# Optimization experiments

Measured on AMD Instinct MI355X. Metric: run time of the kernel, lower is better.

Reference implementation:

```python
import jax, jax.numpy as jnp
import numpy as np

N_NODES = 50000
N_EDGES = 800000


def setup_inputs() -> dict:
    key = jax.random.key(0)
    ks = jax.random.split(key, 16)
    def W(k, shape, fan_in):
        return jax.random.normal(k, shape, dtype=jnp.float32) / np.sqrt(fan_in)
    return {
        "x": jax.random.normal(ks[0], (N_NODES, 64), dtype=jnp.float32),
        "edge_attr": jax.random.uniform(ks[1], (N_EDGES, 1), dtype=jnp.float32),
        "edge_index": jax.random.randint(ks[2], (2, N_EDGES), 0, N_NODES, dtype=jnp.int64),
        "W_pre1": W(ks[3], (65, 16), 65), "b_pre1": jnp.zeros((16,), jnp.float32),
        "W_net1": W(ks[4], (16, 16), 16), "b_net1": jnp.zeros((16,), jnp.float32),
        "W_out1": W(ks[5], (16, 16), 16), "b_out1": jnp.zeros((16,), jnp.float32),
        "W_pre2": W(ks[6], (17, 16), 17), "b_pre2": jnp.zeros((16,), jnp.float32),
        "W_net2": W(ks[7], (16, 16), 16), "b_net2": jnp.zeros((16,), jnp.float32),
        "W_out2": W(ks[8], (16, 16), 16), "b_out2": jnp.zeros((16,), jnp.float32),
    }


def _mpnn_conv(x, edge_index, edge_attr, Wp, bp, Wn, bn, Wo, bo, activation):
    """Edge-gather MLP + scatter-max aggregation (MpnnConv)."""
    src, dst = edge_index[0], edge_index[1]
    # per-edge message: Linear(concat(x_src, edge_attr)) -> relu -> net (Linear)
    m = jnp.concatenate([x[src], edge_attr], axis=1) @ Wp + bp      # [E, mid]
    m = jax.nn.relu(m)
    m = m @ Wn + bn                                                  # [E, mid]
    # scatter-max to destination nodes; empty segments -> 0
    agg = jax.ops.segment_max(m, dst, num_segments=x.shape[0])      # [N, mid]
    agg = jnp.where(jnp.isfinite(agg), agg, 0.0)
    out = agg @ Wo + bo                                              # [N, out]
    return activation(out) if activation is not None else out


def reference(x, edge_attr, edge_index,
              W_pre1, b_pre1, W_net1, b_net1, W_out1, b_out1,
              W_pre2, b_pre2, W_net2, b_net2, W_out2, b_out2):
    # eval mode: dropout is identity
    h = _mpnn_conv(x, edge_index, edge_attr, W_pre1, b_pre1, W_net1, b_net1,
                   W_out1, b_out1, jax.nn.elu)
    h = jax.nn.elu(h)  # outer F.elu in Net.forward
    h = _mpnn_conv(h, edge_index, edge_attr, W_pre2, b_pre2, W_net2, b_net2,
                   W_out2, b_out2, None)
    return jax.nn.log_softmax(h, axis=1)
```

## Files before the change

kernel.cpp:

```cpp
#include <hip/hip_runtime.h>
#include <math.h>

#define NN 50000
#define NE 800000
#define BSHIFT 7
#define BNODES 128
#define NB 391
#define NBB 200
#define EPB 4000
#define PRE_BLOCKS 196

__device__ __forceinline__ float elu1(float v) {
    return v > 0.0f ? v : expm1f(v);
}

__global__ void setup_kernel(const int* __restrict__ ei, int* __restrict__ HM,
                             const float* __restrict__ x,
                             const float* __restrict__ Wp,
                             const float* __restrict__ bp,
                             float* __restrict__ P1) {
    __shared__ unsigned hist[NB];
    __shared__ float sW[64 * 16];
    __shared__ float sb[16];
    if (blockIdx.x < NBB) {
        for (int i = threadIdx.x; i < NB; i += 256) hist[i] = 0;
        __syncthreads();
        int base = blockIdx.x * EPB;
        for (int i = threadIdx.x; i < EPB; i += 256) {
            int d = ei[NE + base + i];
            atomicAdd(&hist[d >> BSHIFT], 1u);
        }
        __syncthreads();
        for (int b = threadIdx.x; b < NB; b += 256)
            HM[b * NBB + blockIdx.x] = (int)hist[b];
    } else {
        for (int i = threadIdx.x; i < 64 * 16; i += 256) sW[i] = Wp[i];
        if (threadIdx.x < 16) sb[threadIdx.x] = bp[threadIdx.x];
        __syncthreads();
        int n = (blockIdx.x - NBB) * 256 + threadIdx.x;
        if (n >= NN) return;
        float acc[16];
#pragma unroll
        for (int k = 0; k < 16; ++k) acc[k] = sb[k];
        const float4* xr = (const float4*)(x + (size_t)n * 64);
#pragma unroll
        for (int j4 = 0; j4 < 16; ++j4) {
            float4 xv = xr[j4];
            const float* w = &sW[j4 * 4 * 16];
#pragma unroll
            for (int k = 0; k < 16; ++k) acc[k] += xv.x * w[k];
#pragma unroll
            for (int k = 0; k < 16; ++k) acc[k] += xv.y * w[16 + k];
#pragma unroll
            for (int k = 0; k < 16; ++k) acc[k] += xv.z * w[32 + k];
#pragma unroll
            for (int k = 0; k < 16; ++k) acc[k] += xv.w * w[48 + k];
        }
        float4* o = (float4*)(P1 + (size_t)n * 16);
        o[0] = make_float4(acc[0], acc[1], acc[2], acc[3]);
        o[1] = make_float4(acc[4], acc[5], acc[6], acc[7]);
        o[2] = make_float4(acc[8], acc[9], acc[10], acc[11]);
        o[3] = make_float4(acc[12], acc[13], acc[14], acc[15]);
    }
}

__global__ void row_scan_kernel(int* __restrict__ HM, int* __restrict__ rowsum) {
    __shared__ int s[256];
    int t = threadIdx.x, b = blockIdx.x;
    int v = (t < NBB) ? HM[b * NBB + t] : 0;
    s[t] = v;
    __syncthreads();
#pragma unroll
    for (int off = 1; off < 256; off <<= 1) {
        int tmp = (t >= off) ? s[t - off] : 0;
        __syncthreads();
        s[t] += tmp;
        __syncthreads();
    }
    if (t < NBB) HM[b * NBB + t] = s[t] - v;
    if (t == 255) rowsum[b] = s[255];
}

__global__ void scan_rows_kernel(const int* __restrict__ rowsum, int* __restrict__ bstart) {
    __shared__ int s[512];
    int t = threadIdx.x;
    int v = (t < NB) ? rowsum[t] : 0;
    s[t] = v;
    __syncthreads();
#pragma unroll
    for (int off = 1; off < 512; off <<= 1) {
        int tmp = (t >= off) ? s[t - off] : 0;
        __syncthreads();
        s[t] += tmp;
        __syncthreads();
    }
    if (t < NB) bstart[t] = s[t] - v;
    if (t == 511) bstart[NB] = s[511];
}

__global__ void bin2_kernel(const int* __restrict__ ei, const float* __restrict__ ea,
                            const int* __restrict__ HM, const int* __restrict__ bstart,
                            int2* __restrict__ sp1) {
    __shared__ unsigned cur[NB];
    for (int b = threadIdx.x; b < NB; b += 256)
        cur[b] = (unsigned)(bstart[b] + HM[b * NBB + blockIdx.x]);
    __syncthreads();
    int base = blockIdx.x * EPB;
    for (int i = threadIdx.x; i < EPB; i += 256) {
        int e = base + i;
        int d = ei[NE + e];
        int srcv = ei[e];
        int b = d >> BSHIFT;
        int dl = d & (BNODES - 1);
        unsigned pos = atomicAdd(&cur[b], 1u);
        sp1[pos] = make_int2(srcv | (dl << 16), __float_as_int(ea[e]));
    }
}

__global__ void sort_kernel(const int2* __restrict__ sp1,
                            const int* __restrict__ bstart,
                            int2* __restrict__ sp2,
                            int* __restrict__ start) {
    __shared__ unsigned hist[BNODES];
    __shared__ unsigned cur[BNODES];
    __shared__ int s[256];
    int tid = threadIdx.x;
    int b = blockIdx.x;
    int e0 = bstart[b], e1 = bstart[b + 1];
    if (tid < BNODES) hist[tid] = 0;
    __syncthreads();
    for (int i = e0 + tid; i < e1; i += 256) {
        int dl = (sp1[i].x >> 16) & (BNODES - 1);
        atomicAdd(&hist[dl], 1u);
    }
    __syncthreads();
    int v = (tid < BNODES) ? (int)hist[tid] : 0;
    s[tid] = v;
    __syncthreads();
#pragma unroll
    for (int off = 1; off < 256; off <<= 1) {
        int t = (tid >= off) ? s[tid - off] : 0;
        __syncthreads();
        s[tid] += t;
        __syncthreads();
    }
    if (tid < BNODES) {
        int excl = s[tid] - v;
        cur[tid] = (unsigned)excl;
        start[b * BNODES + tid] = e0 + excl;
    }
    __syncthreads();
    for (int i = e0 + tid; i < e1; i += 256) {
        int2 rec = sp1[i];
        int dl = (rec.x >> 16) & (BNODES - 1);
        int pos = e0 + (int)atomicAdd(&cur[dl], 1u);
        sp2[pos] = make_int2(rec.x & 0xFFFF, rec.y);
    }
}

template <int MODE>
__global__ void __launch_bounds__(256, 4)
gather_kernel(const long long* __restrict__ sp,
              const int* __restrict__ start,
              const float* __restrict__ Pin,
              const float* __restrict__ wl,
              const float* __restrict__ Wn,
              const float* __restrict__ bn,
              const float* __restrict__ Wo,
              const float* __restrict__ bo,
              const float* __restrict__ Wpn,
              const float* __restrict__ bpn,
              float* __restrict__ out) {
    __shared__ float swl[16], sbn[16], sbo[16], sbpn[16];
    __shared__ float sWnT[16][17];
    __shared__ float sWo[256], sWpn[256];
    __shared__ float sAgg[32][17];
    int tid = threadIdx.x;
    if (tid < 256) {
        sWnT[tid & 15][tid >> 4] = Wn[tid];
        sWo[tid] = Wo[tid];
        if (MODE == 0) sWpn[tid] = Wpn[tid];
    }
    if (tid < 16) {
        swl[tid] = wl[tid]; sbn[tid] = bn[tid]; sbo[tid] = bo[tid];
        if (MODE == 0) sbpn[tid] = bpn[tid];
    }
    __syncthreads();

    int l  = tid >> 3;
    int g  = tid & 3;
    int hi = (tid >> 2) & 1;
    int n = blockIdx.x * 32 + l;
    bool valid = (n < NN);

    float acc[4] = {-INFINITY, -INFINITY, -INFINITY, -INFINITY};
    int s0 = 0, s1 = 0;
    if (valid) { s0 = start[n]; s1 = start[n + 1]; }

    float wl0 = swl[g * 4 + 0], wl1 = swl[g * 4 + 1],
          wl2 = swl[g * 4 + 2], wl3 = swl[g * 4 + 3];
    float bn0 = sbn[g * 4 + 0], bn1 = sbn[g * 4 + 1],
          bn2 = sbn[g * 4 + 2], bn3 = sbn[g * 4 + 3];
    bool g1 = (g & 1) != 0, g2 = (g & 2) != 0;

    float wreg[64];
#pragma unroll
    for (int c = 0; c < 16; ++c) {
#pragma unroll
        for (int j = 0; j < 4; ++j) wreg[c * 4 + j] = sWnT[c][g * 4 + j];
    }

    int s = s0 + hi;
    while (s < s1) {
        int sB = (s + 2 < s1) ? (s + 2) : s;
        long long rA = sp[s];
        long long rB = sp[sB];
        int srcA = (int)(rA & 0xFFFFFFFFll);
        int srcB = (int)(rB & 0xFFFFFFFFll);
        float4 qA = ((const float4*)(Pin + (size_t)srcA * 16))[g];
        float4 qB = ((const float4*)(Pin + (size_t)srcB * 16))[g];
        float aA = __int_as_float((int)(rA >> 32));
        float aB = __int_as_float((int)(rB >> 32));
        s += 4;

#pragma unroll
        for (int e = 0; e < 2; ++e) {
            float4 cv = e ? qB : qA;
            float a = e ? aB : aA;
            float t0 = fmaxf(fmaf(a, wl0, cv.x), 0.0f);
            float t1 = fmaxf(fmaf(a, wl1, cv.y), 0.0f);
            float t2 = fmaxf(fmaf(a, wl2, cv.z), 0.0f);
            float t3 = fmaxf(fmaf(a, wl3, cv.w), 0.0f);
            float m[16];
#pragma unroll
            for (int c = 0; c < 16; ++c) {
                float o = t0 * wreg[c * 4 + 0];
                o = fmaf(t1, wreg[c * 4 + 1], o);
                o = fmaf(t2, wreg[c * 4 + 2], o);
                o = fmaf(t3, wreg[c * 4 + 3], o);
                m[c] = o;
            }
            float h[8];
#pragma unroll
            for (int c = 0; c < 8; ++c) {
                float send = g2 ? m[c] : m[c + 8];
                float recv = __shfl_xor(send, 2, 64);
                h[c] = (g2 ? m[c + 8] : m[c]) + recv;
            }
            float send, recv, r0, r1, r2, r3;
            send = g1 ? h[0] : h[4]; recv = __shfl_xor(send, 1, 64); r0 = (g1 ? h[4] : h[0]) + recv;
            send = g1 ? h[1] : h[5]; recv = __shfl_xor(send, 1, 64); r1 = (g1 ? h[5] : h[1]) + recv;
            send = g1 ? h[2] : h[6]; recv = __shfl_xor(send, 1, 64); r2 = (g1 ? h[6] : h[2]) + recv;
            send = g1 ? h[3] : h[7]; recv = __shfl_xor(send, 1, 64); r3 = (g1 ? h[7] : h[3]) + recv;
            acc[0] = fmaxf(acc[0], r0 + bn0);
            acc[1] = fmaxf(acc[1], r1 + bn1);
            acc[2] = fmaxf(acc[2], r2 + bn2);
            acc[3] = fmaxf(acc[3], r3 + bn3);
        }
    }
#pragma unroll
    for (int q = 0; q < 4; ++q) acc[q] = fmaxf(acc[q], __shfl_xor(acc[q], 4, 64));

    bool empty = (s1 == s0);
#pragma unroll
    for (int q = 0; q < 4; ++q) sAgg[l][g * 4 + q] = empty ? 0.0f : acc[q];
    __syncthreads();

    if (MODE == 0) {
        float h[4];
#pragma unroll
        for (int q = 0; q < 4; ++q) {
            int c = g * 4 + q;
            float o = sbo[c];
#pragma unroll
            for (int j = 0; j < 16; ++j) o = fmaf(sAgg[l][j], sWo[j * 16 + c], o);
            h[q] = elu1(elu1(o));
        }
        __syncthreads();
        if (hi == 0) {
#pragma unroll
            for (int q = 0; q < 4; ++q) sAgg[l][g * 4 + q] = h[q];
        }
        __syncthreads();
        float p[4];
#pragma unroll
        for (int q = 0; q < 4; ++q) {
            int c = g * 4 + q;
            float o = sbpn[c];
#pragma unroll
            for (int k = 0; k < 16; ++k) o = fmaf(sAgg[l][k], sWpn[k * 16 + c], o);
            p[q] = o;
        }
        if (valid && hi == 0) {
            float4* op = (float4*)(out + (size_t)n * 16 + g * 4);
            *op = make_float4(p[0], p[1], p[2], p[3]);
        }
    } else {
        float oo[4];
#pragma unroll
        for (int q = 0; q < 4; ++q) {
            int c = g * 4 + q;
            float o = sbo[c];
#pragma unroll
            for (int j = 0; j < 16; ++j) o = fmaf(sAgg[l][j], sWo[j * 16 + c], o);
            oo[q] = o;
        }
        __syncthreads();
        if (hi == 0) {
#pragma unroll
            for (int q = 0; q < 4; ++q) sAgg[l][g * 4 + q] = oo[q];
        }
        __syncthreads();
        float mx = -INFINITY;
#pragma unroll
        for (int j = 0; j < 16; ++j) mx = fmaxf(mx, sAgg[l][j]);
        float sum = 0.0f;
#pragma unroll
        for (int j = 0; j < 16; ++j) sum += expf(sAgg[l][j] - mx);
        float ls = logf(sum) + mx;
        if (valid && hi == 0) {
            float4* op = (float4*)(out + (size_t)n * 16 + g * 4);
            *op = make_float4(oo[0] - ls, oo[1] - ls, oo[2] - ls, oo[3] - ls);
        }
    }
}

extern "C" void kernel_launch(void* const* d_in, const int* in_sizes, int n_in,
                              void* d_out, int out_size, void* d_ws, size_t ws_size,
                              hipStream_t stream) {
    const float* x         = (const float*)d_in[0];
    const float* edge_attr = (const float*)d_in[1];
    const int*   edge_index= (const int*)  d_in[2];
    const float* W_pre1 = (const float*)d_in[3];
    const float* b_pre1 = (const float*)d_in[4];
    const float* W_net1 = (const float*)d_in[5];
    const float* b_net1 = (const float*)d_in[6];
    const float* W_out1 = (const float*)d_in[7];
    const float* b_out1 = (const float*)d_in[8];
    const float* W_pre2 = (const float*)d_in[9];
    const float* b_pre2 = (const float*)d_in[10];
    const float* W_net2 = (const float*)d_in[11];
    const float* b_net2 = (const float*)d_in[12];
    const float* W_out2 = (const float*)d_in[13];
    const float* b_out2 = (const float*)d_in[14];

    char* ws = (char*)d_ws;
    int2*  sp1    = (int2*) (ws);
    int2*  sp2    = (int2*) (ws + 6400000);
    float* P1     = (float*)(ws + 12800000);
    float* P2     = (float*)(ws + 16000000);
    int*   HM     = (int*)  (ws + 19200000);
    int*   bstart = (int*)  (ws + 19520000);
    int*   rowsum = (int*)  (ws + 19524000);
    int*   start  = (int*)  (ws + 19528000);

    const int GATH_BLOCKS = (NN + 31) / 32;

    setup_kernel<<<NBB + PRE_BLOCKS, 256, 0, stream>>>(edge_index, HM, x, W_pre1, b_pre1, P1);
    row_scan_kernel<<<NB, 256, 0, stream>>>(HM, rowsum);
    scan_rows_kernel<<<1, 512, 0, stream>>>(rowsum, bstart);
    bin2_kernel<<<NBB, 256, 0, stream>>>(edge_index, edge_attr, HM, bstart, sp1);
    sort_kernel<<<NB, 256, 0, stream>>>(sp1, bstart, sp2, start);

    gather_kernel<0><<<GATH_BLOCKS, 256, 0, stream>>>((const long long*)sp2, start, P1,
        W_pre1 + 64 * 16, W_net1, b_net1, W_out1, b_out1, W_pre2, b_pre2, P2);

    gather_kernel<1><<<GATH_BLOCKS, 256, 0, stream>>>((const long long*)sp2, start, P2,
        W_pre2 + 16 * 16, W_net2, b_net2, W_out2, b_out2, nullptr, nullptr,
        (float*)d_out);
}
```

Baseline: 96.67 us.

## Sort nodes by in-degree within each bin to balance gather warp work

The sort kernel now counting-sorts the 128 nodes of each bin by in-degree, capped at 63, and emits a permutation array along with the CSR start offsets in permuted order. The gather kernels then process nodes in that permuted order, so the lanes sharing a wavefront handle nodes with similar edge counts and fewer lanes sit idle in the edge loop. The cost is extra scans and shared-memory work in the sort, one extra indirection load per node in the gather, and output writes that are now scattered by node id.

```diff
diff --git a/kernel.cpp b/kernel.cpp
--- a/kernel.cpp
+++ b/kernel.cpp
@@ -120,40 +120,76 @@
 __global__ void sort_kernel(const int2* __restrict__ sp1,
                             const int* __restrict__ bstart,
                             int2* __restrict__ sp2,
-                            int* __restrict__ start) {
+                            int* __restrict__ start,
+                            int* __restrict__ perm) {
     __shared__ unsigned hist[BNODES];
+    __shared__ int s[256];
+    __shared__ unsigned dcnt[64];
+    __shared__ unsigned dcur[64];
+    __shared__ int dlof[BNODES];
+    __shared__ int soff[BNODES];
     __shared__ unsigned cur[BNODES];
-    __shared__ int s[256];
+    __shared__ int sdeg[BNODES];
     int tid = threadIdx.x;
     int b = blockIdx.x;
     int e0 = bstart[b], e1 = bstart[b + 1];
     if (tid < BNODES) hist[tid] = 0;
+    if (tid < 64) dcnt[tid] = 0;
     __syncthreads();
     for (int i = e0 + tid; i < e1; i += 256) {
         int dl = (sp1[i].x >> 16) & (BNODES - 1);
         atomicAdd(&hist[dl], 1u);
     }
     __syncthreads();
-    int v = (tid < BNODES) ? (int)hist[tid] : 0;
+    if (tid < BNODES) {
+        int key = min((int)hist[tid], 63);
+        atomicAdd(&dcnt[key], 1u);
+    }
+    __syncthreads();
+    int v = (tid < 64) ? (int)dcnt[tid] : 0;
     s[tid] = v;
     __syncthreads();
 #pragma unroll
-    for (int off = 1; off < 256; off <<= 1) {
-        int t = (tid >= off) ? s[tid - off] : 0;
-        __syncthreads();
-        s[tid] += t;
-        __syncthreads();
-    }
+    for (int off = 1; off < 64; off <<= 1) {
+        int tmp = (tid >= off) ? s[tid - off] : 0;
+        __syncthreads();
+        s[tid] += tmp;
+        __syncthreads();
+    }
+    if (tid < 64) dcur[tid] = (unsigned)(s[tid] - v);
+    __syncthreads();
     if (tid < BNODES) {
-        int excl = s[tid] - v;
-        cur[tid] = (unsigned)excl;
-        start[b * BNODES + tid] = e0 + excl;
-    }
+        int key = min((int)hist[tid], 63);
+        int rank = (int)atomicAdd(&dcur[key], 1u);
+        dlof[rank] = tid;
+    }
+    __syncthreads();
+    if (tid < BNODES) sdeg[tid] = (int)hist[dlof[tid]];
+    __syncthreads();
+    int v2 = (tid < BNODES) ? sdeg[tid] : 0;
+    s[tid] = v2;
+    __syncthreads();
+#pragma unroll
+    for (int off = 1; off < 128; off <<= 1) {
+        int tmp = (tid >= off) ? s[tid - off] : 0;
+        __syncthreads();
+        s[tid] += tmp;
+        __syncthreads();
+    }
+    if (tid < BNODES) {
+        int off = s[tid] - v2;
+        soff[tid] = off;
+        start[b * BNODES + tid] = e0 + off;
+        perm[b * BNODES + tid] = b * BNODES + dlof[tid];
+    }
+    __syncthreads();
+    if (tid < BNODES) cur[dlof[tid]] = (unsigned)(e0 + soff[tid]);
+    if (b == NB - 1 && tid == 0) start[NB * BNODES] = e1;
     __syncthreads();
     for (int i = e0 + tid; i < e1; i += 256) {
         int2 rec = sp1[i];
         int dl = (rec.x >> 16) & (BNODES - 1);
-        int pos = e0 + (int)atomicAdd(&cur[dl], 1u);
+        int pos = (int)atomicAdd(&cur[dl], 1u);
         sp2[pos] = make_int2(rec.x & 0xFFFF, rec.y);
     }
 }
@@ -162,6 +198,7 @@
 __global__ void __launch_bounds__(256, 4)
 gather_kernel(const long long* __restrict__ sp,
               const int* __restrict__ start,
+              const int* __restrict__ perm,
               const float* __restrict__ Pin,
               const float* __restrict__ wl,
               const float* __restrict__ Wn,
@@ -190,12 +227,12 @@
     int l  = tid >> 3;
     int g  = tid & 3;
     int hi = (tid >> 2) & 1;
-    int n = blockIdx.x * 32 + l;
+    int r = blockIdx.x * 32 + l;
+    int n = perm[r];
     bool valid = (n < NN);
 
     float acc[4] = {-INFINITY, -INFINITY, -INFINITY, -INFINITY};
-    int s0 = 0, s1 = 0;
-    if (valid) { s0 = start[n]; s1 = start[n + 1]; }
+    int s0 = start[r], s1 = start[r + 1];
 
     float wl0 = swl[g * 4 + 0], wl1 = swl[g * 4 + 1],
           wl2 = swl[g * 4 + 2], wl3 = swl[g * 4 + 3];
@@ -353,19 +390,20 @@
     int*   bstart = (int*)  (ws + 19520000);
     int*   rowsum = (int*)  (ws + 19524000);
     int*   start  = (int*)  (ws + 19528000);
-
-    const int GATH_BLOCKS = (NN + 31) / 32;
+    int*   perm   = (int*)  (ws + 19728256);
+
+    const int GATH_BLOCKS = (NB * BNODES) / 32;
 
     setup_kernel<<<NBB + PRE_BLOCKS, 256, 0, stream>>>(edge_index, HM, x, W_pre1, b_pre1, P1);
     row_scan_kernel<<<NB, 256, 0, stream>>>(HM, rowsum);
     scan_rows_kernel<<<1, 512, 0, stream>>>(rowsum, bstart);
     bin2_kernel<<<NBB, 256, 0, stream>>>(edge_index, edge_attr, HM, bstart, sp1);
-    sort_kernel<<<NB, 256, 0, stream>>>(sp1, bstart, sp2, start);
-
-    gather_kernel<0><<<GATH_BLOCKS, 256, 0, stream>>>((const long long*)sp2, start, P1,
+    sort_kernel<<<NB, 256, 0, stream>>>(sp1, bstart, sp2, start, perm);
+
+    gather_kernel<0><<<GATH_BLOCKS, 256, 0, stream>>>((const long long*)sp2, start, perm, P1,
         W_pre1 + 64 * 16, W_net1, b_net1, W_out1, b_out1, W_pre2, b_pre2, P2);
 
-    gather_kernel<1><<<GATH_BLOCKS, 256, 0, stream>>>((const long long*)sp2, start, P2,
+    gather_kernel<1><<<GATH_BLOCKS, 256, 0, stream>>>((const long long*)sp2, start, perm, P2,
         W_pre2 + 16 * 16, W_net2, b_net2, W_out2, b_out2, nullptr, nullptr,
         (float*)d_out);
 }
```

Measured after the change: 95.50 us. About the same (-1.2%).
